# Performance work log

Measured on AMD Instinct MI355X. Metric: run time of the kernel, lower is better.

## Reference

```python
import jax, jax.numpy as jnp
import numpy as np
from jax import lax

C = 512
BN_EPS = 1e-5
GLN_EPS = 1e-8


def setup_inputs() -> dict:
    key = jax.random.key(0)
    ks = jax.random.split(key, 10)
    B, T = 16, 4000
    x = jax.random.normal(ks[0], (B, C, T), dtype=jnp.float32)
    # BatchNorm1d params (eval mode: affine + running stats)
    bn_gamma = jax.random.normal(ks[1], (C,), dtype=jnp.float32) * 0.1 + 1.0
    bn_beta = jax.random.normal(ks[2], (C,), dtype=jnp.float32) * 0.1
    bn_mean = jax.random.normal(ks[3], (C,), dtype=jnp.float32) * 0.1
    bn_var = jax.random.uniform(ks[4], (C,), dtype=jnp.float32) + 0.5
    # depthwise Conv1d(512,512,3,groups=512,bias=False): kernel [O=C, I=1, K=3]
    dw_w = jax.random.normal(ks[5], (C, 1, 3), dtype=jnp.float32) * (1.0 / np.sqrt(3.0))
    # PReLU default: single shared parameter init 0.25
    prelu_a = jnp.full((1,), 0.25, dtype=jnp.float32)
    # GlobalLayerNorm(512) affine params
    gln_gamma = jnp.ones((C,), dtype=jnp.float32)
    gln_beta = jnp.zeros((C,), dtype=jnp.float32)
    # pointwise Conv1d(512,512,1,bias=False): weight [O, I]
    pw_w = jax.random.normal(ks[6], (C, C), dtype=jnp.float32) * (1.0 / np.sqrt(C))
    return {"x": x, "bn_gamma": bn_gamma, "bn_beta": bn_beta, "bn_mean": bn_mean,
            "bn_var": bn_var, "dw_w": dw_w, "prelu_a": prelu_a,
            "gln_gamma": gln_gamma, "gln_beta": gln_beta, "pw_w": pw_w}


def reference(x, bn_gamma, bn_beta, bn_mean, bn_var, dw_w, prelu_a,
              gln_gamma, gln_beta, pw_w):
    # ReLU
    h = jax.nn.relu(x)
    # BatchNorm1d (eval mode, running stats), per-channel affine over [B,C,T]
    scale = (bn_gamma * lax.rsqrt(bn_var + BN_EPS))[None, :, None]
    h = h * scale + (bn_beta - bn_mean * bn_gamma * lax.rsqrt(bn_var + BN_EPS))[None, :, None]
    # depthwise conv1d, kernel 3, pad 1, groups=C
    h = lax.conv_general_dilated(h, dw_w, window_strides=(1,), padding=((1, 1),),
                                 feature_group_count=C,
                                 dimension_numbers=("NCH", "OIH", "NCH"))
    # PReLU (single shared slope)
    h = jnp.where(h >= 0, h, prelu_a[0] * h)
    # GlobalLayerNorm: normalize over (C, T) per sample, per-channel affine
    mean = jnp.mean(h, axis=(1, 2), keepdims=True)
    var = jnp.mean(jnp.square(h - mean), axis=(1, 2), keepdims=True)
    h = gln_gamma[None, :, None] * (h - mean) * lax.rsqrt(var + GLN_EPS) + gln_beta[None, :, None]
    # pointwise 1x1 conv == channel GEMM
    h = jnp.einsum("oc,bct->bot", pw_w, h)
    # residual
    return h + x
```

## Files before the change

### kernel.cpp

```cpp
#include <hip/hip_runtime.h>
#include <stdint.h>

#define B_ 16
#define C_ 512
#define T_ 4000
#define TPAD 4096

typedef float f32x4 __attribute__((ext_vector_type(4)));
typedef float f32x16 __attribute__((ext_vector_type(16)));
typedef __bf16 bf16x8 __attribute__((ext_vector_type(8)));

__device__ inline unsigned short f2b(float f) {
  uint32_t u = __builtin_bit_cast(uint32_t, f);
  u = (u + 0x7fffu + ((u >> 16) & 1u)) >> 16;
  return (unsigned short)u;
}
__device__ inline float b2f(unsigned short h) {
  uint32_t u = ((uint32_t)h) << 16;
  return __builtin_bit_cast(float, u);
}
__device__ inline void gl_lds16(const void* g, void* s) {
  __builtin_amdgcn_global_load_lds(
      (const __attribute__((address_space(1))) uint32_t*)g,
      (__attribute__((address_space(3))) uint32_t*)s, 16, 0, 0);
}


__global__ void k_init(float* wsf) {
  int i = threadIdx.x;
  if (i < 32) wsf[i] = 0.f;
}

__global__ __launch_bounds__(64) void k_prepw(const float* __restrict__ pw,
                                              const float* __restrict__ gamma,
                                              const float* __restrict__ beta,
                                              unsigned short* __restrict__ Wp,
                                              float* __restrict__ wsf) {
  int o = blockIdx.x, l = threadIdx.x;
  float a1 = 0.f, a2 = 0.f;
  for (int j = 0; j < 8; ++j) {
    int c = j * 64 + l;
    float wv = pw[o * 512 + c];
    unsigned short wb = f2b(wv * gamma[c]);
    Wp[o * 512 + c] = wb;
    a1 += b2f(wb);
    a2 += wv * beta[c];
  }
  for (int s = 32; s > 0; s >>= 1) { a1 += __shfl_down(a1, s); a2 += __shfl_down(a2, s); }
  if (l == 0) { wsf[64 + o] = a1; wsf[576 + o] = a2; }
}

__global__ __launch_bounds__(512) void k_front(const float* __restrict__ x,
    const float* __restrict__ bng, const float* __restrict__ bnb,
    const float* __restrict__ bnm, const float* __restrict__ bnv,
    const float* __restrict__ dw, const float* __restrict__ pa,
    unsigned short* __restrict__ hT, float* __restrict__ wsf) {
  __shared__ unsigned short hs[256 * 128] __attribute__((aligned(16)));
  __shared__ float psc[128], pbi[128], pq0[128], pq1[128], pq2[128];
  __shared__ float partial[16];
  int tid = threadIdx.x;
  int l = tid & 63, w = tid >> 6;
  int tb = blockIdx.x;
  int cb = blockIdx.y;
  int b  = blockIdx.z;
  int t0 = tb * 256;
  if (tid < 128) {
    int c = cb * 128 + tid;
    float sc = bng[c] * rsqrtf(bnv[c] + 1e-5f);
    psc[tid] = sc;
    pbi[tid] = bnb[c] - bnm[c] * sc;
    pq0[tid] = dw[3 * c];
    pq1[tid] = dw[3 * c + 1];
    pq2[tid] = dw[3 * c + 2];
  }
  float alpha = pa[0];
  __syncthreads();

  int t = t0 + 4 * l;
  bool full = (t + 3 < T_);
  bool has_l = (t0 > 0);
  bool has_r = (t0 + 256 < T_);
  float sum = 0.f, sq = 0.f;
  int cs_x = (l & 7) << 3;

#pragma unroll 2
  for (int i = 0; i < 16; ++i) {
    int cl = w * 16 + i;
    const float* xr = x + ((size_t)b * C_ + cb * 128 + cl) * T_;
    float sc = psc[cl], bi = pbi[cl];
    float w0 = pq0[cl], w1 = pq1[cl], w2 = pq2[cl];
    f32x4 u;
    if (full) {
      const f32x4 v = *(const f32x4*)(xr + t);
      u.x = fmaxf(v.x, 0.f) * sc + bi;
      u.y = fmaxf(v.y, 0.f) * sc + bi;
      u.z = fmaxf(v.z, 0.f) * sc + bi;
      u.w = fmaxf(v.w, 0.f) * sc + bi;
    } else {
      u = (f32x4){0.f, 0.f, 0.f, 0.f};
    }
    float el = has_l ? (fmaxf(xr[t0 - 1], 0.f) * sc + bi) : 0.f;
    float er = has_r ? (fmaxf(xr[t0 + 256], 0.f) * sc + bi) : 0.f;
    float up = __shfl_up(u.w, 1);   if (l == 0)  up = el;
    float un = __shfl_down(u.x, 1); if (l == 63) un = er;
    float h[4];
    h[0] = w0 * up  + w1 * u.x + w2 * u.y;
    h[1] = w0 * u.x + w1 * u.y + w2 * u.z;
    h[2] = w0 * u.y + w1 * u.z + w2 * u.w;
    h[3] = w0 * u.z + w1 * u.w + w2 * un;
    int cs = cl ^ cs_x;
#pragma unroll
    for (int j = 0; j < 4; ++j) {
      float p = h[j] >= 0.f ? h[j] : alpha * h[j];
      if (!full) p = 0.f;
      sum += p; sq += p * p;
      hs[(4 * l + j) * 128 + cs] = f2b(p);
    }
  }

  for (int s = 32; s > 0; s >>= 1) { sum += __shfl_down(sum, s); sq += __shfl_down(sq, s); }
  if (l == 0) { partial[w] = sum; partial[8 + w] = sq; }
  __syncthreads();
  if (tid == 0) {
    float a = 0.f, c2 = 0.f;
    for (int k = 0; k < 8; ++k) { a += partial[k]; c2 += partial[8 + k]; }
    atomicAdd(&wsf[b], a);
    atomicAdd(&wsf[16 + b], c2);
  }

  unsigned short* dstb = hT + ((size_t)b * TPAD + t0) * 512 + cb * 128;
#pragma unroll
  for (int p = 0; p < 8; ++p) {
    int idx = p * 512 + tid;
    int tl = idx >> 4, g = idx & 15;
    int gs = g ^ ((tl >> 2) & 7);
    uint4 val = *(const uint4*)(hs + tl * 128 + gs * 8);
    *(uint4*)(dstb + (size_t)tl * 512 + g * 8) = val;
  }
}

__global__ void k_finalize(float* wsf) {
  int b = threadIdx.x;
  if (b < 16) {
    float n = (float)C_ * (float)T_;
    float mean = wsf[b] / n;
    float var = wsf[16 + b] / n - mean * mean;
    wsf[32 + b] = mean;
    wsf[48 + b] = rsqrtf(fmaxf(var, 0.f) + 1e-8f);
  }
}

__global__ __launch_bounds__(512, 4) void k_gemm(const unsigned short* __restrict__ Wp,
    const unsigned short* __restrict__ hT, const float* __restrict__ x,
    const float* __restrict__ wsf, float* __restrict__ out) {
  __shared__ unsigned short Bs[64 * 512] __attribute__((aligned(16)));
  int tid = threadIdx.x;
  int l = tid & 63, w = tid >> 6;
  int nb = blockIdx.x, b = blockIdx.y;
  const unsigned short* hTt = hT + ((size_t)b * TPAD + nb * 64) * 512;

#pragma unroll
  for (int r = 0; r < 8; ++r) {
    int u = r * 512 + tid;
    int row = u >> 6, slot = u & 63;
    gl_lds16(hTt + row * 512 + ((slot ^ (row & 31)) << 3), Bs + u * 8);
  }
  asm volatile("s_waitcnt vmcnt(0)" ::: "memory");
  __syncthreads();

  int o0 = w * 64;
  int lr = l & 31, lh = l >> 5;
  const unsigned short* wpb = Wp + (size_t)(o0 + lr) * 512 + lh * 8;
  const unsigned short* bs0 = Bs + lr * 512;

  f32x16 acc[2][2] = {};
  bf16x8 A0[2][2], A1[2][2];
#pragma unroll
  for (int fm = 0; fm < 2; ++fm)
#pragma unroll
    for (int ks = 0; ks < 2; ++ks)
      A0[fm][ks] = *(const bf16x8*)(wpb + fm * 32 * 512 + ks * 16);

#pragma unroll 1
  for (int kt = 0; kt < 16; kt += 2) {
#pragma unroll
    for (int fm = 0; fm < 2; ++fm)
#pragma unroll
      for (int ks = 0; ks < 2; ++ks)
        A1[fm][ks] = *(const bf16x8*)(wpb + fm * 32 * 512 + (kt + 1) * 32 + ks * 16);
    {
      bf16x8 bv[2][2];
#pragma unroll
      for (int fn = 0; fn < 2; ++fn)
#pragma unroll
        for (int ks = 0; ks < 2; ++ks) {
          int slot = (kt * 4 + ks * 2 + lh) ^ lr;
          bv[fn][ks] = *(const bf16x8*)(bs0 + fn * 32 * 512 + slot * 8);
        }
#pragma unroll
      for (int ks = 0; ks < 2; ++ks)
#pragma unroll
        for (int fm = 0; fm < 2; ++fm)
#pragma unroll
          for (int fn = 0; fn < 2; ++fn)
            acc[fm][fn] = __builtin_amdgcn_mfma_f32_32x32x16_bf16(
                A0[fm][ks], bv[fn][ks], acc[fm][fn], 0, 0, 0);
    }
    if (kt + 2 < 16) {
#pragma unroll
      for (int fm = 0; fm < 2; ++fm)
#pragma unroll
        for (int ks = 0; ks < 2; ++ks)
          A0[fm][ks] = *(const bf16x8*)(wpb + fm * 32 * 512 + (kt + 2) * 32 + ks * 16);
    }
    {
      bf16x8 bv[2][2];
#pragma unroll
      for (int fn = 0; fn < 2; ++fn)
#pragma unroll
        for (int ks = 0; ks < 2; ++ks) {
          int slot = ((kt + 1) * 4 + ks * 2 + lh) ^ lr;
          bv[fn][ks] = *(const bf16x8*)(bs0 + fn * 32 * 512 + slot * 8);
        }
#pragma unroll
      for (int ks = 0; ks < 2; ++ks)
#pragma unroll
        for (int fm = 0; fm < 2; ++fm)
#pragma unroll
          for (int fn = 0; fn < 2; ++fn)
            acc[fm][fn] = __builtin_amdgcn_mfma_f32_32x32x16_bf16(
                A1[fm][ks], bv[fn][ks], acc[fm][fn], 0, 0, 0);
    }
  }

  float mean = wsf[32 + b], rstd = wsf[48 + b];
  float mr = mean * rstd;
#pragma unroll
  for (int fm = 0; fm < 2; ++fm) {
#pragma unroll
    for (int fn = 0; fn < 2; ++fn) {
      int t = nb * 64 + fn * 32 + lr;
      if (t < T_) {
#pragma unroll
        for (int reg = 0; reg < 16; ++reg) {
          int o = o0 + fm * 32 + (reg & 3) + ((reg >> 2) << 3) + (lh << 2);
          float bias = wsf[576 + o] - mr * wsf[64 + o];
          size_t idx = ((size_t)b * C_ + o) * T_ + t;
          out[idx] = rstd * acc[fm][fn][reg] + bias + x[idx];
        }
      }
    }
  }
}

extern "C" void kernel_launch(void* const* d_in, const int* in_sizes, int n_in,
                              void* d_out, int out_size, void* d_ws, size_t ws_size,
                              hipStream_t stream) {
  const float* x   = (const float*)d_in[0];
  const float* bng = (const float*)d_in[1];
  const float* bnb = (const float*)d_in[2];
  const float* bnm = (const float*)d_in[3];
  const float* bnv = (const float*)d_in[4];
  const float* dw  = (const float*)d_in[5];
  const float* pa  = (const float*)d_in[6];
  const float* gg  = (const float*)d_in[7];
  const float* gb  = (const float*)d_in[8];
  const float* pw  = (const float*)d_in[9];
  float* out = (float*)d_out;
  float* wsf = (float*)d_ws;
  unsigned short* Wp = (unsigned short*)((char*)d_ws + 8192);
  unsigned short* hT = (unsigned short*)((char*)d_ws + (1 << 20));

  k_init<<<dim3(1), dim3(64), 0, stream>>>(wsf);
  k_prepw<<<dim3(512), dim3(64), 0, stream>>>(pw, gg, gb, Wp, wsf);
  k_front<<<dim3(16, 4, 16), dim3(512), 0, stream>>>(x, bng, bnb, bnm, bnv, dw, pa, hT, wsf);
  k_finalize<<<dim3(1), dim3(64), 0, stream>>>(wsf);
  k_gemm<<<dim3(64, 16), dim3(512), 0, stream>>>(Wp, hT, x, wsf, out);
}
```

Baseline: 188.6 us.

## Recompute depthwise front inside GEMM instead of materializing bf16 intermediate

The front kernel now only computes the GlobalLayerNorm statistics and no longer writes the transposed bf16 activation tensor. The GEMM kernel re-reads x, recomputes ReLU, BatchNorm, the depthwise conv and PReLU for its 64-timestep tile, and writes the result straight into swizzled LDS. This removes a roughly 64MB write and read of the intermediate, at the cost of reading x twice more and doing a large per-thread register array with scalar strided LDS stores. The grid drops to 63 time blocks, since the padded 64th tile is no longer needed.

```diff
diff --git a/kernel.cpp b/kernel.cpp
--- a/kernel.cpp
+++ b/kernel.cpp
@@ -4,7 +4,6 @@
 #define B_ 16
 #define C_ 512
 #define T_ 4000
-#define TPAD 4096
 
 typedef float f32x4 __attribute__((ext_vector_type(4)));
 typedef float f32x16 __attribute__((ext_vector_type(16)));
@@ -18,11 +17,6 @@
 __device__ inline float b2f(unsigned short h) {
   uint32_t u = ((uint32_t)h) << 16;
   return __builtin_bit_cast(float, u);
-}
-__device__ inline void gl_lds16(const void* g, void* s) {
-  __builtin_amdgcn_global_load_lds(
-      (const __attribute__((address_space(1))) uint32_t*)g,
-      (__attribute__((address_space(3))) uint32_t*)s, 16, 0, 0);
 }
 
 
@@ -50,12 +44,11 @@
   if (l == 0) { wsf[64 + o] = a1; wsf[576 + o] = a2; }
 }
 
-__global__ __launch_bounds__(512) void k_front(const float* __restrict__ x,
+__global__ __launch_bounds__(512) void k_stats(const float* __restrict__ x,
     const float* __restrict__ bng, const float* __restrict__ bnb,
     const float* __restrict__ bnm, const float* __restrict__ bnv,
     const float* __restrict__ dw, const float* __restrict__ pa,
-    unsigned short* __restrict__ hT, float* __restrict__ wsf) {
-  __shared__ unsigned short hs[256 * 128] __attribute__((aligned(16)));
+    float* __restrict__ wsf) {
   __shared__ float psc[128], pbi[128], pq0[128], pq1[128], pq2[128];
   __shared__ float partial[16];
   int tid = threadIdx.x;
@@ -81,7 +74,6 @@
   bool has_l = (t0 > 0);
   bool has_r = (t0 + 256 < T_);
   float sum = 0.f, sq = 0.f;
-  int cs_x = (l & 7) << 3;
 
 #pragma unroll 2
   for (int i = 0; i < 16; ++i) {
@@ -108,13 +100,12 @@
     h[1] = w0 * u.x + w1 * u.y + w2 * u.z;
     h[2] = w0 * u.y + w1 * u.z + w2 * u.w;
     h[3] = w0 * u.z + w1 * u.w + w2 * un;
-    int cs = cl ^ cs_x;
-#pragma unroll
-    for (int j = 0; j < 4; ++j) {
-      float p = h[j] >= 0.f ? h[j] : alpha * h[j];
-      if (!full) p = 0.f;
-      sum += p; sq += p * p;
-      hs[(4 * l + j) * 128 + cs] = f2b(p);
+    if (full) {
+#pragma unroll
+      for (int j = 0; j < 4; ++j) {
+        float p = h[j] >= 0.f ? h[j] : alpha * h[j];
+        sum += p; sq += p * p;
+      }
     }
   }
 
@@ -127,16 +118,6 @@
     atomicAdd(&wsf[b], a);
     atomicAdd(&wsf[16 + b], c2);
   }
-
-  unsigned short* dstb = hT + ((size_t)b * TPAD + t0) * 512 + cb * 128;
-#pragma unroll
-  for (int p = 0; p < 8; ++p) {
-    int idx = p * 512 + tid;
-    int tl = idx >> 4, g = idx & 15;
-    int gs = g ^ ((tl >> 2) & 7);
-    uint4 val = *(const uint4*)(hs + tl * 128 + gs * 8);
-    *(uint4*)(dstb + (size_t)tl * 512 + g * 8) = val;
-  }
 }
 
 __global__ void k_finalize(float* wsf) {
@@ -150,28 +131,57 @@
   }
 }
 
-__global__ __launch_bounds__(512, 4) void k_gemm(const unsigned short* __restrict__ Wp,
-    const unsigned short* __restrict__ hT, const float* __restrict__ x,
+__global__ __launch_bounds__(512, 4) void k_fused(const unsigned short* __restrict__ Wp,
+    const float* __restrict__ x,
+    const float* __restrict__ bng, const float* __restrict__ bnb,
+    const float* __restrict__ bnm, const float* __restrict__ bnv,
+    const float* __restrict__ dw, const float* __restrict__ pa,
     const float* __restrict__ wsf, float* __restrict__ out) {
   __shared__ unsigned short Bs[64 * 512] __attribute__((aligned(16)));
   int tid = threadIdx.x;
+  int nb = blockIdx.x, b = blockIdx.y;
+  int t0 = nb * 64;
+
+  {
+    int c = tid;
+    float sc = bng[c] * rsqrtf(bnv[c] + 1e-5f);
+    float bi = bnb[c] - bnm[c] * sc;
+    float w0 = dw[3 * c], w1 = dw[3 * c + 1], w2 = dw[3 * c + 2];
+    float alpha = pa[0];
+    const float* xr = x + ((size_t)b * C_ + c) * T_;
+    float u[66];
+    u[0] = (t0 > 0) ? fmaxf(xr[t0 - 1], 0.f) * sc + bi : 0.f;
+#pragma unroll
+    for (int ch = 0; ch < 16; ++ch) {
+      int t = t0 + ch * 4;
+      if (t + 3 < T_) {
+        f32x4 v = *(const f32x4*)(xr + t);
+        u[1 + ch * 4 + 0] = fmaxf(v.x, 0.f) * sc + bi;
+        u[1 + ch * 4 + 1] = fmaxf(v.y, 0.f) * sc + bi;
+        u[1 + ch * 4 + 2] = fmaxf(v.z, 0.f) * sc + bi;
+        u[1 + ch * 4 + 3] = fmaxf(v.w, 0.f) * sc + bi;
+      } else {
+#pragma unroll
+        for (int q = 0; q < 4; ++q)
+          u[1 + ch * 4 + q] = (t + q < T_) ? fmaxf(xr[t + q], 0.f) * sc + bi : 0.f;
+      }
+    }
+    u[65] = (t0 + 64 < T_) ? fmaxf(xr[t0 + 64], 0.f) * sc + bi : 0.f;
+    int cslot = c >> 3, clo = c & 7;
+#pragma unroll
+    for (int j = 0; j < 64; ++j) {
+      float h = w0 * u[j] + w1 * u[j + 1] + w2 * u[j + 2];
+      float p = h >= 0.f ? h : alpha * h;
+      if (t0 + j >= T_) p = 0.f;
+      Bs[j * 512 + ((cslot ^ (j & 31)) << 3) + clo] = f2b(p);
+    }
+  }
+  __syncthreads();
+
   int l = tid & 63, w = tid >> 6;
-  int nb = blockIdx.x, b = blockIdx.y;
-  const unsigned short* hTt = hT + ((size_t)b * TPAD + nb * 64) * 512;
-
-#pragma unroll
-  for (int r = 0; r < 8; ++r) {
-    int u = r * 512 + tid;
-    int row = u >> 6, slot = u & 63;
-    gl_lds16(hTt + row * 512 + ((slot ^ (row & 31)) << 3), Bs + u * 8);
-  }
-  asm volatile("s_waitcnt vmcnt(0)" ::: "memory");
-  __syncthreads();
-
   int o0 = w * 64;
   int lr = l & 31, lh = l >> 5;
   const unsigned short* wpb = Wp + (size_t)(o0 + lr) * 512 + lh * 8;
-  const unsigned short* bs0 = Bs + lr * 512;
 
   f32x16 acc[2][2] = {};
   bf16x8 A0[2][2], A1[2][2];
@@ -195,7 +205,7 @@
 #pragma unroll
         for (int ks = 0; ks < 2; ++ks) {
           int slot = (kt * 4 + ks * 2 + lh) ^ lr;
-          bv[fn][ks] = *(const bf16x8*)(bs0 + fn * 32 * 512 + slot * 8);
+          bv[fn][ks] = *(const bf16x8*)(Bs + (fn * 32 + lr) * 512 + slot * 8);
         }
 #pragma unroll
       for (int ks = 0; ks < 2; ++ks)
@@ -220,7 +230,7 @@
 #pragma unroll
         for (int ks = 0; ks < 2; ++ks) {
           int slot = ((kt + 1) * 4 + ks * 2 + lh) ^ lr;
-          bv[fn][ks] = *(const bf16x8*)(bs0 + fn * 32 * 512 + slot * 8);
+          bv[fn][ks] = *(const bf16x8*)(Bs + (fn * 32 + lr) * 512 + slot * 8);
         }
 #pragma unroll
       for (int ks = 0; ks < 2; ++ks)
@@ -239,7 +249,7 @@
   for (int fm = 0; fm < 2; ++fm) {
 #pragma unroll
     for (int fn = 0; fn < 2; ++fn) {
-      int t = nb * 64 + fn * 32 + lr;
+      int t = t0 + fn * 32 + lr;
       if (t < T_) {
 #pragma unroll
         for (int reg = 0; reg < 16; ++reg) {
@@ -269,11 +279,10 @@
   float* out = (float*)d_out;
   float* wsf = (float*)d_ws;
   unsigned short* Wp = (unsigned short*)((char*)d_ws + 8192);
-  unsigned short* hT = (unsigned short*)((char*)d_ws + (1 << 20));
 
   k_init<<<dim3(1), dim3(64), 0, stream>>>(wsf);
   k_prepw<<<dim3(512), dim3(64), 0, stream>>>(pw, gg, gb, Wp, wsf);
-  k_front<<<dim3(16, 4, 16), dim3(512), 0, stream>>>(x, bng, bnb, bnm, bnv, dw, pa, hT, wsf);
+  k_stats<<<dim3(16, 4, 16), dim3(512), 0, stream>>>(x, bng, bnb, bnm, bnv, dw, pa, wsf);
   k_finalize<<<dim3(1), dim3(64), 0, stream>>>(wsf);
-  k_gemm<<<dim3(64, 16), dim3(512), 0, stream>>>(Wp, hT, x, wsf, out);
-}
+  k_fused<<<dim3(63, 16), dim3(512), 0, stream>>>(Wp, x, bng, bnb, bnm, bnv, dw, pa, wsf, out);
+}
```

Result: slower. 220.2 us (+16.8%).
